# Kernel tuning notes

Hardware: AMD Instinct MI355X
Metric: run time of the kernel (lower is better)

Reference implementation:

```python
import jax, jax.numpy as jnp
import numpy as np

D_EMB = 1024
N_HEAD = 16
D_K = D_EMB // N_HEAD


def setup_inputs() -> dict:
    key = jax.random.key(0)
    ks = jax.random.split(key, 11)
    B, S = 2, 2048
    s = 1.0 / np.sqrt(D_EMB)
    inp = {
        'Q': jax.random.normal(ks[0], (B, S, D_EMB), jnp.float32),
        'K': jax.random.normal(ks[1], (B, S, D_EMB), jnp.float32),
        'V': jax.random.normal(ks[2], (B, S, D_EMB), jnp.float32),
        'W_Q': jax.random.normal(ks[3], (D_EMB, D_EMB), jnp.float32) * s,
        'b_Q': jax.random.normal(ks[4], (D_EMB,), jnp.float32) * s,
        'W_K': jax.random.normal(ks[5], (D_EMB, D_EMB), jnp.float32) * s,
        'b_K': jax.random.normal(ks[6], (D_EMB,), jnp.float32) * s,
        'W_V': jax.random.normal(ks[7], (D_EMB, D_EMB), jnp.float32) * s,
        'b_V': jax.random.normal(ks[8], (D_EMB,), jnp.float32) * s,
        'W_O': jax.random.normal(ks[9], (D_EMB, D_EMB), jnp.float32) * s,
        'b_O': jax.random.normal(ks[10], (D_EMB,), jnp.float32) * s,
    }
    return inp


def _heads(x):
    # [B, S, D] -> [B, H, S, d_k]
    B, S, _ = x.shape
    return x.reshape(B, S, N_HEAD, D_K).transpose(0, 2, 1, 3)


def reference(Q, K, V, W_Q, b_Q, W_K, b_K, W_V, b_V, W_O, b_O):
    q = _heads(Q @ W_Q.T + b_Q)
    k = _heads(K @ W_K.T + b_K)
    v = _heads(V @ W_V.T + b_V)
    scale = 1.0 / jnp.sqrt(jnp.asarray(D_K, q.dtype))
    scores = jnp.einsum('bhqd,bhkd->bhqk', q, k) * scale  # [B,H,S,S]
    probs = jax.nn.softmax(scores, axis=-1)
    attn = jnp.einsum('bhqk,bhkd->bhqd', probs, v)
    B, H, S, d = attn.shape
    attn = attn.transpose(0, 2, 1, 3).reshape(B, S, H * d)
    return attn @ W_O.T + b_O
```

## Files before the change

kernel.cpp:

```cpp
#include <hip/hip_runtime.h>
#include <cstdint>
#include <cstddef>

#define S_LEN 2048
#define NH    16
#define DKH   64
#define DEMB  1024
#define MTOT  4096
#define SLAB  (32 * S_LEN * DKH)

typedef float f32x4 __attribute__((ext_vector_type(4)));
typedef __bf16 bf16x8 __attribute__((ext_vector_type(8)));
typedef _Float16 f16;
typedef f16 f16x2 __attribute__((ext_vector_type(2)));
typedef f16 f16x4 __attribute__((ext_vector_type(4)));
typedef f16 f16x8 __attribute__((ext_vector_type(8)));
typedef unsigned short u16;
typedef unsigned int u32;
typedef u16 u16x8 __attribute__((ext_vector_type(8)));
typedef u16 u16x4 __attribute__((ext_vector_type(4)));
typedef u32 u32x4 __attribute__((ext_vector_type(4)));

static __device__ __forceinline__ u16 f2bf(float f) {
  u32 u = __builtin_bit_cast(u32, f);
  u += 0x7fffu + ((u >> 16) & 1u);
  return (u16)(u >> 16);
}
static __device__ __forceinline__ float bf2f(u16 b) {
  return __builtin_bit_cast(float, ((u32)b) << 16);
}
static __device__ __forceinline__ bf16x8 ldfrag(const u16* p) {
  return __builtin_bit_cast(bf16x8, *(const u16x8*)p);
}
static __device__ __forceinline__ f16x8 ldfragh8(const u16* p) {
  return __builtin_bit_cast(f16x8, *(const u16x8*)p);
}
static __device__ __forceinline__ f32x4 mfma16(bf16x8 a, bf16x8 b, f32x4 c) {
  return __builtin_amdgcn_mfma_f32_16x16x32_bf16(a, b, c, 0, 0, 0);
}
static __device__ __forceinline__ f32x4 mfmah32(f16x8 a, f16x8 b, f32x4 c) {
  return __builtin_amdgcn_mfma_f32_16x16x32_f16(a, b, c, 0, 0, 0);
}
static __device__ __forceinline__ void gl2lds16(const void* g, void* l) {
  __builtin_amdgcn_global_load_lds((__attribute__((address_space(1))) void*)g,
                                   (__attribute__((address_space(3))) void*)l,
                                   16, 0, 0);
}
static __device__ __forceinline__ u32 pkh2(float a, float b) {
  return __builtin_bit_cast(u32, __builtin_amdgcn_cvt_pkrtz(a, b));
}
static __device__ __forceinline__ f16x4 pkh4(float a, float b, float c, float d) {
  f16x2 lo = __builtin_bit_cast(f16x2, __builtin_amdgcn_cvt_pkrtz(a, b));
  f16x2 hi = __builtin_bit_cast(f16x2, __builtin_amdgcn_cvt_pkrtz(c, d));
  return __builtin_shufflevector(lo, hi, 0, 1, 2, 3);
}

#define SCL_Q (0.125f * 1.44269504088896340736f)

__global__ __launch_bounds__(256) void cvt_all(
    const float* __restrict__ wq, const float* __restrict__ wk,
    const float* __restrict__ wv, const float* __restrict__ wo,
    const float* __restrict__ q, const float* __restrict__ k,
    const float* __restrict__ v, u16* __restrict__ dW, u16* __restrict__ dA) {
  int b = blockIdx.x;
  const float* s; u16* d;
  if (b < 4096) {
    const int seg = b >> 10;
    s = (seg == 0) ? wq : (seg == 1) ? wk : (seg == 2) ? wv : wo;
    d = dW + (size_t)seg * (DEMB * DEMB);
    b &= 1023;
  } else {
    const int bb = b - 4096;
    const int seg = bb >> 12;
    s = (seg == 0) ? q : (seg == 1) ? k : v;
    d = dA + (size_t)seg * ((size_t)MTOT * DEMB);
    b = bb & 4095;
  }
  const int i = (b * 256 + threadIdx.x) * 4;
  f32x4 f = *(const f32x4*)(s + i);
  u16x4 o;
  o[0] = f2bf(f[0]); o[1] = f2bf(f[1]); o[2] = f2bf(f[2]); o[3] = f2bf(f[3]);
  *(u16x4*)(d + i) = o;
}

__global__ __launch_bounds__(256) void qkv_gemm(
    const u16* __restrict__ qin, const u16* __restrict__ kin,
    const u16* __restrict__ vin, const u16* __restrict__ W,
    const float* __restrict__ bq, const float* __restrict__ bk,
    const float* __restrict__ bv,
    u16* __restrict__ qh, u16* __restrict__ kh, u16* __restrict__ vt) {
  __shared__ __align__(16) u16 sA[128 * 64];
  __shared__ __align__(16) u16 sB[128 * 64];
  const int t = threadIdx.x;
  const int l = t & 63, w = t >> 6;
  const int ll = l & 15, lg = l >> 4;
  const int nb = blockIdx.x;
  const int mb = blockIdx.y;
  const int which = nb >> 3;
  const u16* A = (which == 0) ? qin : ((which == 1) ? kin : vin);
  const int wr = (w >> 1) * 64, wc = (w & 1) * 64;

  f32x4 acc[4][4] = {};

  for (int kt = 0; kt < 16; ++kt) {
    const int k0 = kt * 64;
    __syncthreads();
#pragma unroll
    for (int i = 0; i < 4; ++i) {
      const int c = i * 256 + t;
      const int row = c >> 3;
      const int gc = (c & 7) ^ (row & 7);
      gl2lds16(A + (size_t)(mb * 128 + row) * DEMB + k0 + gc * 8, &sA[c * 8]);
      gl2lds16(W + (size_t)(nb * 128 + row) * DEMB + k0 + gc * 8, &sB[c * 8]);
    }
    __syncthreads();

#pragma unroll
    for (int kk = 0; kk < 2; ++kk) {
      bf16x8 af[4], bfr[4];
#pragma unroll
      for (int i2 = 0; i2 < 4; ++i2) {
        const int row = wr + i2 * 16 + ll;
        af[i2] = ldfrag(&sA[row * 64 + ((kk * 4 + lg) ^ (row & 7)) * 8]);
      }
#pragma unroll
      for (int j2 = 0; j2 < 4; ++j2) {
        const int row = wc + j2 * 16 + ll;
        bfr[j2] = ldfrag(&sB[row * 64 + ((kk * 4 + lg) ^ (row & 7)) * 8]);
      }
#pragma unroll
      for (int i2 = 0; i2 < 4; ++i2)
#pragma unroll
        for (int j2 = 0; j2 < 4; ++j2)
          acc[i2][j2] = mfma16(af[i2], bfr[j2], acc[i2][j2]);
    }
  }

  const float* bias = (which == 0) ? bq : ((which == 1) ? bk : bv);
  const int b = (mb * 128) >> 11;

  if (which == 2) {
#pragma unroll
    for (int j2 = 0; j2 < 4; ++j2) {
      const int nl = (nb * 128 + wc + j2 * 16 + ll) & 1023;
      const int h = nl >> 6, dk = nl & 63;
      const float bb = bias[nl];
      u16* base = vt + ((size_t)((b * NH + h) * DKH + dk)) * S_LEN;
#pragma unroll
      for (int i2 = 0; i2 < 4; ++i2) {
        const int s = (mb * 128 + wr + i2 * 16 + lg * 4) & 2047;
        const f16x4 pk = pkh4(acc[i2][j2][0] + bb, acc[i2][j2][1] + bb,
                              acc[i2][j2][2] + bb, acc[i2][j2][3] + bb);
        *(u16x4*)&base[s] = __builtin_bit_cast(u16x4, pk);
      }
    }
  } else {
    u16* outp = (which == 0) ? qh : kh;
    const float scl = (which == 0) ? SCL_Q : 1.0f;
#pragma unroll
    for (int j2 = 0; j2 < 4; ++j2) {
      const int nl = (nb * 128 + wc + j2 * 16 + ll) & 1023;
      const int h = nl >> 6, dk = nl & 63;
      const float bb = bias[nl];
#pragma unroll
      for (int i2 = 0; i2 < 4; ++i2) {
#pragma unroll
        for (int r = 0; r < 4; ++r) {
          const int s = (mb * 128 + wr + i2 * 16 + lg * 4 + r) & 2047;
          const float val = (acc[i2][j2][r] + bb) * scl;
          outp[((size_t)((b * NH + h) * S_LEN + s)) * DKH + dk] = f2bf(val);
        }
      }
    }
  }
}

__global__ __launch_bounds__(512, 4) void attn_kernel(
    const u16* __restrict__ qh, const u16* __restrict__ kh,
    const u16* __restrict__ vt, u16* __restrict__ opart,
    float* __restrict__ lpart) {
  __shared__ __align__(16) u16 sK0[64 * 64], sK1[64 * 64];
  __shared__ __align__(16) u16 sV0[64 * 64], sV1[64 * 64];
  const int t = threadIdx.x;
  const int l = t & 63, w = t >> 6;
  const int ll = l & 15, lg = l >> 4;
  const int qb = blockIdx.x >> 1;
  const int ks = blockIdx.x & 1;
  const int q_blk = qb * 256;
  const int bh = blockIdx.y;

  bf16x8 aq[2][2];
#pragma unroll
  for (int qt = 0; qt < 2; ++qt) {
    const u16* qbase =
        qh + ((size_t)bh * S_LEN + q_blk + w * 32 + qt * 16 + ll) * DKH;
    aq[qt][0] = ldfrag(qbase + lg * 8);
    aq[qt][1] = ldfrag(qbase + 32 + lg * 8);
  }

  f32x4 oT[2][4] = {};
  float l_part[2] = {0.f, 0.f};

  const int strow = t >> 3;
  const int sgc = (t & 7) ^ (strow & 7);
  const u16* kstg =
      kh + ((size_t)bh * S_LEN + ks * 1024 + strow) * DKH + sgc * 8;
  const u16* vstg =
      vt + ((size_t)bh * DKH + strow) * S_LEN + ks * 1024 + sgc * 8;

  auto stg = [&](int kt, u16* dK, u16* dV) {
    gl2lds16(kstg + (size_t)kt * 64 * DKH, dK + t * 8);
    gl2lds16(vstg + kt * 64, dV + t * 8);
  };

  auto compute = [&](const u16* cK, const u16* cV) {
#pragma unroll
    for (int pr = 0; pr < 2; ++pr) {
      u32 pw0[4], pw1[4];
#pragma unroll
      for (int h = 0; h < 2; ++h) {
        const int krow = (pr * 2 + h) * 16 + ll;
        const bf16x8 ak0 = ldfrag(&cK[krow * 64 + (lg ^ (ll & 7)) * 8]);
        const bf16x8 ak1 = ldfrag(&cK[krow * 64 + ((4 + lg) ^ (ll & 7)) * 8]);
        f32x4 s0 = {}, s1 = {};
        s0 = mfma16(ak0, aq[0][0], s0);
        s0 = mfma16(ak1, aq[0][1], s0);
        s1 = mfma16(ak0, aq[1][0], s1);
        s1 = mfma16(ak1, aq[1][1], s1);
        {
          const float p0 = __builtin_amdgcn_exp2f(s0[0]);
          const float p1 = __builtin_amdgcn_exp2f(s0[1]);
          const float p2 = __builtin_amdgcn_exp2f(s0[2]);
          const float p3 = __builtin_amdgcn_exp2f(s0[3]);
          l_part[0] += (p0 + p1) + (p2 + p3);
          if (h == 0) { pw0[0] = pkh2(p0, p1); pw0[1] = pkh2(p2, p3); }
          else        { pw0[2] = pkh2(p0, p1); pw0[3] = pkh2(p2, p3); }
        }
        {
          const float p0 = __builtin_amdgcn_exp2f(s1[0]);
          const float p1 = __builtin_amdgcn_exp2f(s1[1]);
          const float p2 = __builtin_amdgcn_exp2f(s1[2]);
          const float p3 = __builtin_amdgcn_exp2f(s1[3]);
          l_part[1] += (p0 + p1) + (p2 + p3);
          if (h == 0) { pw1[0] = pkh2(p0, p1); pw1[1] = pkh2(p2, p3); }
          else        { pw1[2] = pkh2(p0, p1); pw1[3] = pkh2(p2, p3); }
        }
      }
      asm volatile("v_permlane32_swap_b32 %0, %1" : "+v"(pw0[0]), "+v"(pw0[2]));
      asm volatile("v_permlane16_swap_b32 %0, %1" : "+v"(pw0[0]), "+v"(pw0[2]));
      asm volatile("v_permlane32_swap_b32 %0, %1" : "+v"(pw0[1]), "+v"(pw0[3]));
      asm volatile("v_permlane16_swap_b32 %0, %1" : "+v"(pw0[1]), "+v"(pw0[3]));
      asm volatile("v_permlane32_swap_b32 %0, %1" : "+v"(pw1[0]), "+v"(pw1[2]));
      asm volatile("v_permlane16_swap_b32 %0, %1" : "+v"(pw1[0]), "+v"(pw1[2]));
      asm volatile("v_permlane32_swap_b32 %0, %1" : "+v"(pw1[1]), "+v"(pw1[3]));
      asm volatile("v_permlane16_swap_b32 %0, %1" : "+v"(pw1[1]), "+v"(pw1[3]));
      const f16x8 bp0 =
          __builtin_bit_cast(f16x8, (u32x4){pw0[0], pw0[1], pw0[2], pw0[3]});
      const f16x8 bp1 =
          __builtin_bit_cast(f16x8, (u32x4){pw1[0], pw1[1], pw1[2], pw1[3]});

#pragma unroll
      for (int nt = 0; nt < 4; ++nt) {
        const int row = nt * 16 + ll;
        const f16x8 av =
            ldfragh8(&cV[row * 64 + ((pr * 4 + lg) ^ (ll & 7)) * 8]);
        oT[0][nt] = mfmah32(av, bp0, oT[0][nt]);
        oT[1][nt] = mfmah32(av, bp1, oT[1][nt]);
      }
    }
  };

  stg(0, sK0, sV0);
  __syncthreads();
  for (int kt2 = 0; kt2 < 8; ++kt2) {
    stg(2 * kt2 + 1, sK1, sV1);
    compute(sK0, sV0);
    __syncthreads();
    if (kt2 < 7) stg(2 * kt2 + 2, sK0, sV0);
    compute(sK1, sV1);
    __syncthreads();
  }

#pragma unroll
  for (int qt = 0; qt < 2; ++qt) {
    float lv = l_part[qt];
    lv += __shfl_xor(lv, 16, 64);
    lv += __shfl_xor(lv, 32, 64);
    const int orow = q_blk + w * 32 + qt * 16 + ll;
    u16* obase = opart + (((size_t)(ks * 32 + bh)) * S_LEN + orow) * DKH;
#pragma unroll
    for (int nt = 0; nt < 4; ++nt) {
      u16x4 o;
#pragma unroll
      for (int r = 0; r < 4; ++r) o[r] = f2bf(oT[qt][nt][r]);
      *(u16x4*)&obase[nt * 16 + lg * 4] = o;
    }
    if (lg == 0) lpart[(ks * 32 + bh) * S_LEN + orow] = lv;
  }
}

__global__ __launch_bounds__(256) void merge_ctx(
    const u16* __restrict__ op, const float* __restrict__ lp,
    u16* __restrict__ ctx) {
  const int idx = blockIdx.x * 256 + threadIdx.x;
  const int dk8 = idx & 7;
  const int q = (idx >> 3) & 2047;
  const int bh = idx >> 14;
  const float inv = 1.0f / (lp[bh * S_LEN + q] + lp[(32 + bh) * S_LEN + q]);
  const u16x8 a = *(const u16x8*)&op[((size_t)bh * S_LEN + q) * DKH + dk8 * 8];
  const u16x8 c = *(const u16x8*)&op[((size_t)(32 + bh) * S_LEN + q) * DKH + dk8 * 8];
  u16x8 o;
#pragma unroll
  for (int r = 0; r < 8; ++r) o[r] = f2bf((bf2f(a[r]) + bf2f(c[r])) * inv);
  const int b = bh >> 4, h = bh & 15;
  *(u16x8*)&ctx[((size_t)((b * S_LEN + q) * NH + h)) * DKH + dk8 * 8] = o;
}

__global__ __launch_bounds__(256) void out_gemm(
    const u16* __restrict__ Am, const u16* __restrict__ W,
    const float* __restrict__ bo, float* __restrict__ out) {
  __shared__ __align__(16) u16 sA0[128 * 64], sA1[128 * 64];
  __shared__ __align__(16) u16 sB0[64 * 64], sB1[64 * 64];
  const int t = threadIdx.x;
  const int l = t & 63, w = t >> 6;
  const int ll = l & 15, lg = l >> 4;
  const int nb = blockIdx.x;
  const int mb = blockIdx.y;
  const int wr = (w >> 1) * 64, wc = (w & 1) * 32;

  f32x4 acc[4][2] = {};

  auto stg = [&](int kt, u16* dA, u16* dB) {
    const int k0 = kt * 64;
#pragma unroll
    for (int i = 0; i < 4; ++i) {
      const int c = i * 256 + t;
      const int row = c >> 3;
      const int gc = (c & 7) ^ (row & 7);
      gl2lds16(Am + (size_t)(mb * 128 + row) * DEMB + k0 + gc * 8, dA + c * 8);
      if (i < 2)
        gl2lds16(W + (size_t)(nb * 64 + row) * DEMB + k0 + gc * 8, dB + c * 8);
    }
  };

  auto comp = [&](const u16* cA, const u16* cB) {
#pragma unroll
    for (int kk = 0; kk < 2; ++kk) {
      bf16x8 af[4], bfr[2];
#pragma unroll
      for (int i2 = 0; i2 < 4; ++i2) {
        const int row = wr + i2 * 16 + ll;
        af[i2] = ldfrag(&cA[row * 64 + ((kk * 4 + lg) ^ (row & 7)) * 8]);
      }
#pragma unroll
      for (int j2 = 0; j2 < 2; ++j2) {
        const int row = wc + j2 * 16 + ll;
        bfr[j2] = ldfrag(&cB[row * 64 + ((kk * 4 + lg) ^ (row & 7)) * 8]);
      }
#pragma unroll
      for (int i2 = 0; i2 < 4; ++i2)
#pragma unroll
        for (int j2 = 0; j2 < 2; ++j2)
          acc[i2][j2] = mfma16(af[i2], bfr[j2], acc[i2][j2]);
    }
  };

  stg(0, sA0, sB0);
  __syncthreads();
  for (int kt2 = 0; kt2 < 8; ++kt2) {
    stg(2 * kt2 + 1, sA1, sB1);
    comp(sA0, sB0);
    __syncthreads();
    if (kt2 < 7) stg(2 * kt2 + 2, sA0, sB0);
    comp(sA1, sB1);
    __syncthreads();
  }

#pragma unroll
  for (int j2 = 0; j2 < 2; ++j2) {
    const int ncol = nb * 64 + wc + j2 * 16 + ll;
    const float bb = bo[ncol];
#pragma unroll
    for (int i2 = 0; i2 < 4; ++i2) {
#pragma unroll
      for (int r = 0; r < 4; ++r) {
        const int mrow = mb * 128 + wr + i2 * 16 + lg * 4 + r;
        out[(size_t)mrow * DEMB + ncol] = acc[i2][j2][r] + bb;
      }
    }
  }
}

extern "C" void kernel_launch(void* const* d_in, const int* in_sizes, int n_in,
                              void* d_out, int out_size, void* d_ws,
                              size_t ws_size, hipStream_t stream) {
  (void)in_sizes; (void)n_in; (void)out_size; (void)ws_size;
  const float* Q  = (const float*)d_in[0];
  const float* K  = (const float*)d_in[1];
  const float* V  = (const float*)d_in[2];
  const float* WQ = (const float*)d_in[3];
  const float* bQ = (const float*)d_in[4];
  const float* WK = (const float*)d_in[5];
  const float* bK = (const float*)d_in[6];
  const float* WV = (const float*)d_in[7];
  const float* bV = (const float*)d_in[8];
  const float* WO = (const float*)d_in[9];
  const float* bO = (const float*)d_in[10];
  float* out = (float*)d_out;

  u16* ws   = (u16*)d_ws;
  u16* Wqkv = ws;
  u16* Wo   = Wqkv + 3072 * 1024;
  u16* qin  = Wo + 1024 * 1024;
  u16* kin  = qin + (size_t)MTOT * DEMB;
  u16* vin  = kin + (size_t)MTOT * DEMB;
  u16* qh   = vin + (size_t)MTOT * DEMB;
  u16* kh   = qh + 32 * 2048 * 64;
  u16* vt   = kh + 32 * 2048 * 64;
  u16* ctx  = vt + 32 * 2048 * 64;
  u16* opart   = qin;
  float* lpart = (float*)Wqkv;

  cvt_all<<<16384, 256, 0, stream>>>(WQ, WK, WV, WO, Q, K, V, Wqkv, qin);

  qkv_gemm<<<dim3(24, 32), 256, 0, stream>>>(qin, kin, vin, Wqkv, bQ, bK, bV,
                                             qh, kh, vt);
  attn_kernel<<<dim3(16, 32), 512, 0, stream>>>(qh, kh, vt, opart, lpart);
  merge_ctx<<<2048, 256, 0, stream>>>(opart, lpart, ctx);
  out_gemm<<<dim3(16, 32), 256, 0, stream>>>(ctx, Wo, bO, out);
}
```

Baseline: 222.7 us.

## Double-buffer QKV GEMM LDS tiles and remap blocks for XCD locality

The QKV projection GEMM now stages K-tiles of 32 into two LDS buffers, issuing the next tile's global-to-LDS loads before computing on the current one. This overlaps memory traffic with MFMA work and drops one barrier per step. Block indices are also remapped so each XCD handles a contiguous group of M blocks, which should improve L2 reuse of the A rows. The swizzle changes to fit 32-wide rows, and the shorter K-step means more barriers overall.

```diff
diff --git a/kernel.cpp b/kernel.cpp
--- a/kernel.cpp
+++ b/kernel.cpp
@@ -89,51 +89,61 @@
     const float* __restrict__ bq, const float* __restrict__ bk,
     const float* __restrict__ bv,
     u16* __restrict__ qh, u16* __restrict__ kh, u16* __restrict__ vt) {
-  __shared__ __align__(16) u16 sA[128 * 64];
-  __shared__ __align__(16) u16 sB[128 * 64];
+  __shared__ __align__(16) u16 sA0[128 * 32], sA1[128 * 32];
+  __shared__ __align__(16) u16 sB0[128 * 32], sB1[128 * 32];
   const int t = threadIdx.x;
   const int l = t & 63, w = t >> 6;
   const int ll = l & 15, lg = l >> 4;
-  const int nb = blockIdx.x;
-  const int mb = blockIdx.y;
+  const int orig = blockIdx.x + 24 * blockIdx.y;
+  const int xcd = orig & 7, q = orig >> 3;
+  const int nb = q >> 2;
+  const int mb = xcd * 4 + (q & 3);
   const int which = nb >> 3;
   const u16* A = (which == 0) ? qin : ((which == 1) ? kin : vin);
   const int wr = (w >> 1) * 64, wc = (w & 1) * 64;
 
   f32x4 acc[4][4] = {};
 
-  for (int kt = 0; kt < 16; ++kt) {
-    const int k0 = kt * 64;
-    __syncthreads();
-#pragma unroll
-    for (int i = 0; i < 4; ++i) {
+  auto stg = [&](int kt, u16* dA, u16* dB) {
+    const int k0 = kt * 32;
+#pragma unroll
+    for (int i = 0; i < 2; ++i) {
       const int c = i * 256 + t;
-      const int row = c >> 3;
-      const int gc = (c & 7) ^ (row & 7);
-      gl2lds16(A + (size_t)(mb * 128 + row) * DEMB + k0 + gc * 8, &sA[c * 8]);
-      gl2lds16(W + (size_t)(nb * 128 + row) * DEMB + k0 + gc * 8, &sB[c * 8]);
-    }
-    __syncthreads();
-
-#pragma unroll
-    for (int kk = 0; kk < 2; ++kk) {
-      bf16x8 af[4], bfr[4];
-#pragma unroll
-      for (int i2 = 0; i2 < 4; ++i2) {
-        const int row = wr + i2 * 16 + ll;
-        af[i2] = ldfrag(&sA[row * 64 + ((kk * 4 + lg) ^ (row & 7)) * 8]);
-      }
-#pragma unroll
-      for (int j2 = 0; j2 < 4; ++j2) {
-        const int row = wc + j2 * 16 + ll;
-        bfr[j2] = ldfrag(&sB[row * 64 + ((kk * 4 + lg) ^ (row & 7)) * 8]);
-      }
-#pragma unroll
-      for (int i2 = 0; i2 < 4; ++i2)
-#pragma unroll
-        for (int j2 = 0; j2 < 4; ++j2)
-          acc[i2][j2] = mfma16(af[i2], bfr[j2], acc[i2][j2]);
-    }
+      const int row = c >> 2;
+      const int gc = (c & 3) ^ ((row >> 1) & 3);
+      gl2lds16(A + (size_t)(mb * 128 + row) * DEMB + k0 + gc * 8, dA + c * 8);
+      gl2lds16(W + (size_t)(nb * 128 + row) * DEMB + k0 + gc * 8, dB + c * 8);
+    }
+  };
+
+  auto comp = [&](const u16* cA, const u16* cB) {
+    bf16x8 af[4], bfr[4];
+#pragma unroll
+    for (int i2 = 0; i2 < 4; ++i2) {
+      const int row = wr + i2 * 16 + ll;
+      af[i2] = ldfrag(&cA[row * 32 + (lg ^ ((row >> 1) & 3)) * 8]);
+    }
+#pragma unroll
+    for (int j2 = 0; j2 < 4; ++j2) {
+      const int row = wc + j2 * 16 + ll;
+      bfr[j2] = ldfrag(&cB[row * 32 + (lg ^ ((row >> 1) & 3)) * 8]);
+    }
+#pragma unroll
+    for (int i2 = 0; i2 < 4; ++i2)
+#pragma unroll
+      for (int j2 = 0; j2 < 4; ++j2)
+        acc[i2][j2] = mfma16(af[i2], bfr[j2], acc[i2][j2]);
+  };
+
+  stg(0, sA0, sB0);
+  __syncthreads();
+  for (int kt2 = 0; kt2 < 16; ++kt2) {
+    stg(2 * kt2 + 1, sA1, sB1);
+    comp(sA0, sB0);
+    __syncthreads();
+    if (kt2 < 15) stg(2 * kt2 + 2, sA0, sB0);
+    comp(sA1, sB1);
+    __syncthreads();
   }
 
   const float* bias = (which == 0) ? bq : ((which == 1) ? bk : bv);
```

New measurement: 222.6 us. No clear change (-0.0%).
